# Performance work log

Hardware: AMD Instinct MI355X
Metric: run time of the kernel (lower is better)

Reference implementation:

```python
import jax, jax.numpy as jnp
import numpy as np

B, L, D = 2, 2048, 2048
H, KV, HD = 16, 8, 128
EPS = 1e-5
ROPE_BASE = 10000.0
SCALING_ALPHA = 1.0
SCALE = HD ** -0.5


def setup_inputs() -> dict:
    key = jax.random.key(0)
    ks = jax.random.split(key, 5)
    s = 0.02  # weight init scale
    return {
        "x": jax.random.normal(ks[0], (B, L, D), jnp.float32),
        "wq": jax.random.normal(ks[1], (D, H * HD), jnp.float32) * s,
        "wk": jax.random.normal(ks[2], (D, KV * HD), jnp.float32) * s,
        "wv": jax.random.normal(ks[3], (D, KV * HD), jnp.float32) * s,
        "wo": jax.random.normal(ks[4], (H * HD, D), jnp.float32) * s,
        "qn_w": jnp.ones((HD,), jnp.float32),
        "kn_w": jnp.ones((HD,), jnp.float32),
    }


def _rope(t):
    # t: [B, h, L, HD]. DynamicNTKAlpha base scaling (alpha=1 -> no-op).
    base = ROPE_BASE * SCALING_ALPHA ** (HD / (HD - 2))
    # NOTE: source uses base**(+i/d) (no negative exponent) -- kept faithful.
    freqs = base ** (jnp.arange(0, HD, 2, dtype=jnp.float32) / HD)  # [HD/2]
    pos = jnp.arange(t.shape[-2], dtype=jnp.float32)                # [L]
    angles = pos[:, None] * freqs[None, :]                          # [L, HD/2]
    cos, sin = jnp.cos(angles), jnp.sin(angles)
    x1, x2 = t[..., : HD // 2], t[..., HD // 2 :]
    return jnp.concatenate([x1 * cos - x2 * sin, x2 * cos + x1 * sin], axis=-1)


def _rmsnorm(t, w):
    return t * jax.lax.rsqrt(jnp.mean(t * t, axis=-1, keepdims=True) + EPS) * w


def reference(x, wq, wk, wv, wo, qn_w, kn_w):
    b, l, _ = x.shape
    q = (x @ wq).reshape(b, l, H, HD).transpose(0, 2, 1, 3)   # [B,H,L,HD]
    k = (x @ wk).reshape(b, l, KV, HD).transpose(0, 2, 1, 3)  # [B,KV,L,HD]
    v = (x @ wv).reshape(b, l, KV, HD).transpose(0, 2, 1, 3)
    q = _rmsnorm(_rope(q), qn_w)
    k = _rmsnorm(_rope(k), kn_w)
    # GQA: expand KV heads to match query heads
    rep = H // KV
    k = jnp.repeat(k, rep, axis=1)  # [B,H,L,HD]
    v = jnp.repeat(v, rep, axis=1)
    scores = jnp.einsum("bhqd,bhkd->bhqk", q, k) * SCALE
    probs = jax.nn.softmax(scores, axis=-1)
    out = jnp.einsum("bhqk,bhkd->bhqd", probs, v)             # [B,H,L,HD]
    out = out.transpose(0, 2, 1, 3).reshape(b, l, H * HD)
    return out @ wo
```

## Files before the change

kernel.cpp:

```cpp
#include <hip/hip_runtime.h>
#include <math.h>

#define BB 2
#define LL 2048
#define DD 2048
#define HH 16
#define KVH 8
#define HDIM 128
#define SCALE_F 0.08838834764831845f
#define EPS_F 1e-5f
#define LOG2E 1.4426950408889634f
#define SMAX_F 17.0f
#define QKVW 4096

typedef unsigned short u16;
typedef __attribute__((ext_vector_type(8))) short short8;
typedef __attribute__((ext_vector_type(4))) float f32x4;
typedef __attribute__((ext_vector_type(16))) float f32x16;

#define MFMA16(a, b, c) __builtin_amdgcn_mfma_f32_16x16x32_bf16((a), (b), (c), 0, 0, 0)
#define MFMA32(a, b, c) __builtin_amdgcn_mfma_f32_32x32x16_bf16((a), (b), (c), 0, 0, 0)

__device__ __forceinline__ float b2f(u16 u) {
    union { unsigned int i; float f; } x;
    x.i = ((unsigned int)u) << 16;
    return x.f;
}
__device__ __forceinline__ u16 f2b(float f) {
    unsigned int x = __float_as_uint(f);
    unsigned int r = x + 0x7FFFu + ((x >> 16) & 1u);
    return (u16)(r >> 16);
}
__device__ __forceinline__ unsigned cvtpk(float lo, float hi) {
    unsigned r;
    asm("v_cvt_pk_bf16_f32 %0, %1, %2" : "=v"(r) : "v"(lo), "v"(hi));
    return r;
}
__device__ __forceinline__ void pl32swap(unsigned &a, unsigned &b) {
    asm("v_permlane32_swap_b32 %0, %1" : "+v"(a), "+v"(b));
}
__device__ __forceinline__ void g2l(const u16* g, u16* l) {
    __builtin_amdgcn_global_load_lds(
        (const __attribute__((address_space(1))) unsigned int*)g,
        (__attribute__((address_space(3))) unsigned int*)l, 16, 0, 0);
}

__global__ __launch_bounds__(256) void prep_kernel(const float* __restrict__ x,
                                                   u16* __restrict__ xb,
                                                   const float* __restrict__ wq,
                                                   const float* __restrict__ wk,
                                                   const float* __restrict__ wv,
                                                   const float* __restrict__ wo,
                                                   u16* __restrict__ wqkvT,
                                                   u16* __restrict__ woT,
                                                   float* __restrict__ ct,
                                                   float* __restrict__ st) {
    __shared__ u16 t[64 * 65];
    const int blk = blockIdx.x, tid = threadIdx.x;
    if (blk < 8192) {
        int i = (blk * 256 + tid) * 4;
        float4 v = *(const float4*)(x + i);
        unsigned int p0 = (unsigned int)f2b(v.x) | ((unsigned int)f2b(v.y) << 16);
        unsigned int p1 = (unsigned int)f2b(v.z) | ((unsigned int)f2b(v.w) << 16);
        uint2 pk; pk.x = p0; pk.y = p1;
        *(uint2*)(xb + i) = pk;
    } else if (blk < 11264) {
        int j = blk - 8192;
        const float* in; u16* out; int C, bx, by;
        if (j < 1024)      { in = wq; out = wqkvT;                      C = 2048; bx = j & 31; by = j >> 5; }
        else if (j < 1536) { j -= 1024; in = wk; out = wqkvT + (size_t)2048 * DD; C = 1024; bx = j & 15; by = j >> 4; }
        else if (j < 2048) { j -= 1536; in = wv; out = wqkvT + (size_t)3072 * DD; C = 1024; bx = j & 15; by = j >> 4; }
        else               { j -= 2048; in = wo; out = woT;                      C = 2048; bx = j & 31; by = j >> 5; }
        int c0 = bx * 64, r0 = by * 64;
#pragma unroll
        for (int i = 0; i < 16; i++) {
            int idx = tid + i * 256;
            int r = idx >> 6, c = idx & 63;
            t[r * 65 + c] = f2b(in[(size_t)(r0 + r) * C + c0 + c]);
        }
        __syncthreads();
#pragma unroll
        for (int i = 0; i < 16; i++) {
            int idx = tid + i * 256;
            int r = idx >> 6, c = idx & 63;
            out[(size_t)(c0 + r) * DD + r0 + c] = t[c * 65 + r];
        }
    } else {
        int i = (blk - 11264) * 256 + tid;
        int pos = i >> 6, d = i & 63;
        float freq = (float)pow(10000.0, (double)d * (1.0 / 64.0));
        float ang = (float)pos * freq;
        double a = (double)ang;
        ct[i] = (float)cos(a);
        st[i] = (float)sin(a);
    }
}

__global__ __launch_bounds__(256) void gemm_bt(const u16* __restrict__ A,
                                               const u16* __restrict__ Bt,
                                               u16* __restrict__ C, int M, int N, int K) {
    __shared__ __align__(16) u16 As[128 * 64];
    __shared__ __align__(16) u16 Bs[128 * 64];
    const int tid = threadIdx.x;
    const int w = tid >> 6, lane = tid & 63;
    const int lm = lane & 15, lq = lane >> 4;
    const int bn0 = blockIdx.x * 128, bm0 = blockIdx.y * 128;
    const int wm = (w >> 1) * 64, wn = (w & 1) * 64;

    f32x4 acc[4][4];
#pragma unroll
    for (int i = 0; i < 4; i++)
#pragma unroll
        for (int j = 0; j < 4; j++) acc[i][j] = (f32x4){0.f, 0.f, 0.f, 0.f};

    const int srow = lane >> 3;
    const int sgr = (lane & 7) ^ (srow & 7);
    const u16* ga = A + (size_t)(bm0 + w * 32 + srow) * K + sgr * 8;
    const u16* gb = Bt + (size_t)(bn0 + w * 32 + srow) * K + sgr * 8;
    u16* lA = &As[(w * 32) * 64];
    u16* lB = &Bs[(w * 32) * 64];

    for (int k0 = 0; k0 < K; k0 += 64) {
        __syncthreads();
#pragma unroll
        for (int ch = 0; ch < 4; ch++)
            g2l(ga + (size_t)(ch * 8) * K + k0, lA + ch * 8 * 64);
#pragma unroll
        for (int ch = 0; ch < 4; ch++)
            g2l(gb + (size_t)(ch * 8) * K + k0, lB + ch * 8 * 64);
        __syncthreads();

#pragma unroll
        for (int sub = 0; sub < 2; sub++) {
            short8 af[4], bf[4];
#pragma unroll
            for (int mt = 0; mt < 4; mt++) {
                int row = wm + mt * 16 + lm;
                af[mt] = *(const short8*)(&As[row * 64 + ((sub * 4 + lq) ^ (lm & 7)) * 8]);
            }
#pragma unroll
            for (int nt = 0; nt < 4; nt++) {
                int row = wn + nt * 16 + lm;
                bf[nt] = *(const short8*)(&Bs[row * 64 + ((sub * 4 + lq) ^ (lm & 7)) * 8]);
            }
#pragma unroll
            for (int mt = 0; mt < 4; mt++)
#pragma unroll
                for (int nt = 0; nt < 4; nt++) acc[mt][nt] = MFMA16(af[mt], bf[nt], acc[mt][nt]);
        }
    }

#pragma unroll
    for (int mt = 0; mt < 4; mt++)
#pragma unroll
        for (int nt = 0; nt < 4; nt++)
#pragma unroll
            for (int r = 0; r < 4; r++) {
                int row = bm0 + wm + mt * 16 + lq * 4 + r;
                int col = bn0 + wn + nt * 16 + lm;
                C[(size_t)row * N + col] = f2b(acc[mt][nt][r]);
            }
}

__global__ __launch_bounds__(256) void gemm_bt_o(const u16* __restrict__ A,
                                                 const u16* __restrict__ Bt,
                                                 float* __restrict__ C, int M, int N, int K) {
    __shared__ __align__(16) u16 As[64 * 64];
    __shared__ __align__(16) u16 Bs[128 * 64];
    const int tid = threadIdx.x;
    const int w = tid >> 6, lane = tid & 63;
    const int lm = lane & 15, lq = lane >> 4;
    const int bn0 = blockIdx.x * 128, bm0 = blockIdx.y * 64;
    const int wm = (w >> 1) * 32, wn = (w & 1) * 64;

    f32x4 acc[2][4];
#pragma unroll
    for (int i = 0; i < 2; i++)
#pragma unroll
        for (int j = 0; j < 4; j++) acc[i][j] = (f32x4){0.f, 0.f, 0.f, 0.f};

    const int srow = lane >> 3;
    const int sgr = (lane & 7) ^ (srow & 7);
    const u16* ga = A + (size_t)(bm0 + w * 16 + srow) * K + sgr * 8;
    const u16* gb = Bt + (size_t)(bn0 + w * 32 + srow) * K + sgr * 8;
    u16* lA = &As[(w * 16) * 64];
    u16* lB = &Bs[(w * 32) * 64];

    for (int k0 = 0; k0 < K; k0 += 64) {
        __syncthreads();
#pragma unroll
        for (int ch = 0; ch < 2; ch++)
            g2l(ga + (size_t)(ch * 8) * K + k0, lA + ch * 8 * 64);
#pragma unroll
        for (int ch = 0; ch < 4; ch++)
            g2l(gb + (size_t)(ch * 8) * K + k0, lB + ch * 8 * 64);
        __syncthreads();

#pragma unroll
        for (int sub = 0; sub < 2; sub++) {
            short8 af[2], bf[4];
#pragma unroll
            for (int mt = 0; mt < 2; mt++) {
                int row = wm + mt * 16 + lm;
                af[mt] = *(const short8*)(&As[row * 64 + ((sub * 4 + lq) ^ (lm & 7)) * 8]);
            }
#pragma unroll
            for (int nt = 0; nt < 4; nt++) {
                int row = wn + nt * 16 + lm;
                bf[nt] = *(const short8*)(&Bs[row * 64 + ((sub * 4 + lq) ^ (lm & 7)) * 8]);
            }
#pragma unroll
            for (int mt = 0; mt < 2; mt++)
#pragma unroll
                for (int nt = 0; nt < 4; nt++) acc[mt][nt] = MFMA16(af[mt], bf[nt], acc[mt][nt]);
        }
    }

#pragma unroll
    for (int mt = 0; mt < 2; mt++)
#pragma unroll
        for (int nt = 0; nt < 4; nt++)
#pragma unroll
            for (int r = 0; r < 4; r++) {
                int row = bm0 + wm + mt * 16 + lq * 4 + r;
                int col = bn0 + wn + nt * 16 + lm;
                C[(size_t)row * N + col] = acc[mt][nt][r];
            }
}

__global__ __launch_bounds__(256) void ropetv_kernel(u16* __restrict__ qkv,
                                                     u16* __restrict__ vt,
                                                     const float* __restrict__ qw,
                                                     const float* __restrict__ kw,
                                                     const float* __restrict__ ct,
                                                     const float* __restrict__ st) {
    __shared__ u16 t[64 * 65];
    const int blk = blockIdx.x, tid = threadIdx.x;
    if (blk < 24576) {
        int slot = blk * 4 + (tid >> 6);
        int lane = tid & 63;
        int hh = slot % (HH + KVH);
        int row = slot / (HH + KVH);
        int pos = row & (LL - 1);

        u16* base = qkv + (size_t)row * QKVW + hh * HDIM;
        const float* w = (hh < HH) ? qw : kw;

        float x1 = b2f(base[lane]), x2 = b2f(base[lane + 64]);
        float c = ct[pos * 64 + lane], s = st[pos * 64 + lane];
        float r1 = x1 * c - x2 * s;
        float r2 = x2 * c + x1 * s;
        float ss = r1 * r1 + r2 * r2;
#pragma unroll
        for (int m = 1; m < 64; m <<= 1) ss += __shfl_xor(ss, m, 64);
        float sc = 1.0f / sqrtf(ss * (1.0f / 128.0f) + EPS_F);
        base[lane] = f2b(r1 * sc * w[lane]);
        base[lane + 64] = f2b(r2 * sc * w[lane + 64]);
    } else {
        int j = blk - 24576;
        int bx = j & 31, by = (j >> 5) & 1, bg = j >> 6;
        int l0 = bx * 64, d0 = by * 64;
        int b = bg >> 3, g = bg & 7;
        const u16* src = qkv + (size_t)b * LL * QKVW + 3072 + g * HDIM;
        u16* dst = vt + (size_t)bg * HDIM * LL;
#pragma unroll
        for (int i = 0; i < 16; i++) {
            int idx = tid + i * 256;
            int r = idx >> 6, c = idx & 63;
            t[r * 65 + c] = src[(size_t)(l0 + r) * QKVW + d0 + c];
        }
        __syncthreads();
#pragma unroll
        for (int i = 0; i < 16; i++) {
            int idx = tid + i * 256;
            int r = idx >> 6, c = idx & 63;
            dst[(size_t)(d0 + r) * LL + l0 + c] = t[c * 65 + r];
        }
    }
}

__global__ __launch_bounds__(256, 2) void attn_kernel(const u16* __restrict__ qkv,
                                                      const u16* __restrict__ vt,
                                                      u16* __restrict__ ob) {
    __shared__ __align__(16) u16 Kt[2][64 * 128];
    __shared__ __align__(16) u16 Vt[2][128 * 64];

    const int tid = threadIdx.x, w = tid >> 6, lane = tid & 63;
    const int l31 = lane & 31, lh = lane >> 5;
    const int q0 = blockIdx.x * 128;
    const int bh = blockIdx.y, b = bh >> 4, hd = bh & 15, g = hd >> 1;

    const u16* kbase = qkv + (size_t)b * LL * QKVW + 2048 + g * HDIM;
    const u16* vtbase = vt + (size_t)(b * KVH + g) * HDIM * LL;

    const int krl = lane >> 4, kgl = lane & 15;
    const int vrl = lane >> 3, vgl = lane & 7;

#define STAGE(tt, bi) do {                                                   \
        _Pragma("unroll")                                                    \
        for (int ch = 0; ch < 4; ch++) {                                     \
            int r_ = w * 16 + ch * 4 + krl;                                  \
            int gc_ = kgl ^ (r_ & 15);                                       \
            g2l(kbase + (size_t)((tt) * 64 + r_) * QKVW + gc_ * 8,           \
                &Kt[bi][(w * 16 + ch * 4) * 128]);                           \
        }                                                                    \
        _Pragma("unroll")                                                    \
        for (int ch = 0; ch < 4; ch++) {                                     \
            int r_ = w * 32 + ch * 8 + vrl;                                  \
            int gc_ = vgl ^ (r_ & 7);                                        \
            g2l(vtbase + (size_t)r_ * LL + (tt) * 64 + gc_ * 8,              \
                &Vt[bi][(w * 32 + ch * 8) * 64]);                            \
        }                                                                    \
    } while (0)

    const int qrow = q0 + w * 32 + l31;
    short8 aq[8];
    {
        const u16* qp = qkv + (size_t)(b * LL + qrow) * QKVW + hd * HDIM + lh * 8;
#pragma unroll
        for (int kk = 0; kk < 8; kk++) aq[kk] = *(const short8*)(qp + kk * 16);
    }

    f32x16 o[4];
#pragma unroll
    for (int i = 0; i < 4; i++)
#pragma unroll
        for (int r = 0; r < 16; r++) o[i][r] = 0.f;
    float psum = 0.f;
    const float SC2 = SCALE_F * LOG2E;

    STAGE(0, 0);
    __syncthreads();

    int cur = 0;
    for (int t = 0; t < LL / 64; t++) {
        if (t + 1 < LL / 64) STAGE(t + 1, cur ^ 1);

        f32x16 s[2];
#pragma unroll
        for (int kt = 0; kt < 2; kt++)
#pragma unroll
            for (int r = 0; r < 16; r++) s[kt][r] = 0.f;
        __builtin_amdgcn_s_setprio(1);
#pragma unroll
        for (int kk = 0; kk < 8; kk++) {
#pragma unroll
            for (int kt = 0; kt < 2; kt++) {
                int key = kt * 32 + l31;
                int gg = (kk * 2 + lh) ^ (key & 15);
                short8 kf = *(const short8*)(&Kt[cur][key * 128 + gg * 8]);
                s[kt] = MFMA32(kf, aq[kk], s[kt]);
            }
        }
        __builtin_amdgcn_s_setprio(0);

        unsigned pw[4][4];
#pragma unroll
        for (int kt = 0; kt < 2; kt++) {
            float p[16];
#pragma unroll
            for (int r = 0; r < 16; r++) {
                p[r] = exp2f(fmaf(s[kt][r], SC2, -SMAX_F));
                psum += p[r];
            }
#pragma unroll
            for (int half = 0; half < 2; half++) {
                int kc = kt * 2 + half, qb = half * 8;
                unsigned c0 = cvtpk(p[qb + 0], p[qb + 1]);
                unsigned c1 = cvtpk(p[qb + 2], p[qb + 3]);
                unsigned c2 = cvtpk(p[qb + 4], p[qb + 5]);
                unsigned c3 = cvtpk(p[qb + 6], p[qb + 7]);
                pl32swap(c0, c2);
                pl32swap(c1, c3);
                pw[kc][0] = c0; pw[kc][1] = c1; pw[kc][2] = c2; pw[kc][3] = c3;
            }
        }

        __builtin_amdgcn_s_setprio(1);
#pragma unroll
        for (int kc = 0; kc < 4; kc++) {
            union { unsigned u[4]; short8 s8; } pu;
#pragma unroll
            for (int i = 0; i < 4; i++) pu.u[i] = pw[kc][i];
#pragma unroll
            for (int dn = 0; dn < 4; dn++) {
                int d = dn * 32 + l31;
                int gv = ((kc * 2 + lh) ^ (d & 7)) * 8;
                short8 bv = *(const short8*)(&Vt[cur][d * 64 + gv]);
                o[dn] = MFMA32(pu.s8, bv, o[dn]);
            }
        }
        __builtin_amdgcn_s_setprio(0);

        __syncthreads();
        cur ^= 1;
    }
#undef STAGE

    psum += __shfl_xor(psum, 32, 64);
    float inv = 1.0f / psum;
    float invr[16];
#pragma unroll
    for (int r = 0; r < 16; r++) {
        int row = (r & 3) + 8 * (r >> 2) + 4 * lh;
        invr[r] = __shfl(inv, row, 32);
    }

    u16* obase = ob + (size_t)(b * LL + q0 + w * 32) * (HH * HDIM) + hd * HDIM;
#pragma unroll
    for (int dn = 0; dn < 4; dn++)
#pragma unroll
        for (int r = 0; r < 16; r++) {
            int row = (r & 3) + 8 * (r >> 2) + 4 * lh;
            obase[(size_t)row * (HH * HDIM) + dn * 32 + l31] = f2b(o[dn][r] * invr[r]);
        }
}

extern "C" void kernel_launch(void* const* d_in, const int* in_sizes, int n_in,
                              void* d_out, int out_size, void* d_ws, size_t ws_size,
                              hipStream_t stream) {
    const float* x  = (const float*)d_in[0];
    const float* wq = (const float*)d_in[1];
    const float* wk = (const float*)d_in[2];
    const float* wv = (const float*)d_in[3];
    const float* wo = (const float*)d_in[4];
    const float* qn = (const float*)d_in[5];
    const float* kn = (const float*)d_in[6];

    u16* ws = (u16*)d_ws;
    const size_t SZ_X = (size_t)BB * LL * DD;
    u16* xb    = ws;
    u16* qkv   = xb + SZ_X;
    u16* wqkvT = qkv + (size_t)BB * LL * QKVW;
    u16* woT   = wqkvT + (size_t)QKVW * DD;
    float* ct  = (float*)(woT + (size_t)DD * DD);
    float* st  = ct + (size_t)LL * 64;
    u16* att = xb;
    u16* vt  = wqkvT;

    prep_kernel<<<dim3(11776), dim3(256), 0, stream>>>(x, xb, wq, wk, wv, wo,
                                                       wqkvT, woT, ct, st);
    gemm_bt<<<dim3(QKVW / 128, BB * LL / 128), dim3(256), 0, stream>>>(xb, wqkvT, qkv, BB * LL, QKVW, DD);
    ropetv_kernel<<<dim3(25600), dim3(256), 0, stream>>>(qkv, vt, qn, kn, ct, st);
    attn_kernel<<<dim3(LL / 128, BB * HH), dim3(256), 0, stream>>>(qkv, vt, att);
    gemm_bt_o<<<dim3(DD / 128, BB * LL / 64), dim3(256), 0, stream>>>(att, woT, (float*)d_out, BB * LL, DD, DD);
}
```

Measured before the change: 362.7 us.

## Split attention key tiles across warps with 64-query blocks and merge partial outputs

The attention kernel now processes 64 query rows per block instead of 128. Warps are split into two query halves and two key halves, and each warp computes one 32-key subtile. The partial outputs and row sums are combined through shared memory at the end. V is now single-buffered while K stays double-buffered, with explicit vmcnt waits and barriers, which cuts shared memory so three blocks can fit per CU and doubles the grid. The cost is an extra in-block barrier per tile, a final reduction through LDS, and reloading K and V for twice as many blocks.

```diff
diff --git a/kernel.cpp b/kernel.cpp
--- a/kernel.cpp
+++ b/kernel.cpp
@@ -279,15 +279,16 @@
     }
 }
 
-__global__ __launch_bounds__(256, 2) void attn_kernel(const u16* __restrict__ qkv,
+__global__ __launch_bounds__(256, 3) void attn_kernel(const u16* __restrict__ qkv,
                                                       const u16* __restrict__ vt,
                                                       u16* __restrict__ ob) {
-    __shared__ __align__(16) u16 Kt[2][64 * 128];
-    __shared__ __align__(16) u16 Vt[2][128 * 64];
+    __shared__ __align__(16) u16 SM[2 * 64 * 128 + 128 * 64];
+    u16* Vt = SM + 2 * 64 * 128;
 
     const int tid = threadIdx.x, w = tid >> 6, lane = tid & 63;
     const int l31 = lane & 31, lh = lane >> 5;
-    const int q0 = blockIdx.x * 128;
+    const int qh = w & 1, kh = w >> 1;
+    const int q0 = blockIdx.x * 64;
     const int bh = blockIdx.y, b = bh >> 4, hd = bh & 15, g = hd >> 1;
 
     const u16* kbase = qkv + (size_t)b * LL * QKVW + 2048 + g * HDIM;
@@ -296,24 +297,26 @@
     const int krl = lane >> 4, kgl = lane & 15;
     const int vrl = lane >> 3, vgl = lane & 7;
 
-#define STAGE(tt, bi) do {                                                   \
+#define STAGEK(tt, bi) do {                                                  \
         _Pragma("unroll")                                                    \
         for (int ch = 0; ch < 4; ch++) {                                     \
             int r_ = w * 16 + ch * 4 + krl;                                  \
             int gc_ = kgl ^ (r_ & 15);                                       \
             g2l(kbase + (size_t)((tt) * 64 + r_) * QKVW + gc_ * 8,           \
-                &Kt[bi][(w * 16 + ch * 4) * 128]);                           \
+                SM + (bi) * 8192 + (w * 16 + ch * 4) * 128);                 \
         }                                                                    \
+    } while (0)
+#define STAGEV(tt) do {                                                      \
         _Pragma("unroll")                                                    \
         for (int ch = 0; ch < 4; ch++) {                                     \
             int r_ = w * 32 + ch * 8 + vrl;                                  \
             int gc_ = vgl ^ (r_ & 7);                                        \
             g2l(vtbase + (size_t)r_ * LL + (tt) * 64 + gc_ * 8,              \
-                &Vt[bi][(w * 32 + ch * 8) * 64]);                            \
+                Vt + (w * 32 + ch * 8) * 64);                                \
         }                                                                    \
     } while (0)
 
-    const int qrow = q0 + w * 32 + l31;
+    const int qrow = q0 + qh * 32 + l31;
     short8 aq[8];
     {
         const u16* qp = qkv + (size_t)(b * LL + qrow) * QKVW + hd * HDIM + lh * 8;
@@ -328,92 +331,114 @@
         for (int r = 0; r < 16; r++) o[i][r] = 0.f;
     float psum = 0.f;
     const float SC2 = SCALE_F * LOG2E;
-
-    STAGE(0, 0);
-    __syncthreads();
-
-    int cur = 0;
+    const f32x16 fz = {};
+
+    STAGEK(0, 0);
+    asm volatile("s_waitcnt vmcnt(0)" ::: "memory");
+    __builtin_amdgcn_s_barrier();
+
     for (int t = 0; t < LL / 64; t++) {
-        if (t + 1 < LL / 64) STAGE(t + 1, cur ^ 1);
-
-        f32x16 s[2];
-#pragma unroll
-        for (int kt = 0; kt < 2; kt++)
-#pragma unroll
-            for (int r = 0; r < 16; r++) s[kt][r] = 0.f;
+        const int cur = t & 1;
+        const u16* Kc = SM + cur * 8192;
+        STAGEV(t);
+        STAGEK((t + 1) & (LL / 64 - 1), cur ^ 1);
+
+        const int key = kh * 32 + l31;
+        f32x16 s;
         __builtin_amdgcn_s_setprio(1);
-#pragma unroll
-        for (int kk = 0; kk < 8; kk++) {
-#pragma unroll
-            for (int kt = 0; kt < 2; kt++) {
-                int key = kt * 32 + l31;
-                int gg = (kk * 2 + lh) ^ (key & 15);
-                short8 kf = *(const short8*)(&Kt[cur][key * 128 + gg * 8]);
-                s[kt] = MFMA32(kf, aq[kk], s[kt]);
-            }
+        {
+            int gg = lh ^ (key & 15);
+            short8 kf = *(const short8*)(&Kc[key * 128 + gg * 8]);
+            s = MFMA32(kf, aq[0], fz);
+        }
+#pragma unroll
+        for (int kk = 1; kk < 8; kk++) {
+            int gg = (kk * 2 + lh) ^ (key & 15);
+            short8 kf = *(const short8*)(&Kc[key * 128 + gg * 8]);
+            s = MFMA32(kf, aq[kk], s);
         }
         __builtin_amdgcn_s_setprio(0);
 
-        unsigned pw[4][4];
-#pragma unroll
-        for (int kt = 0; kt < 2; kt++) {
-            float p[16];
-#pragma unroll
-            for (int r = 0; r < 16; r++) {
-                p[r] = exp2f(fmaf(s[kt][r], SC2, -SMAX_F));
-                psum += p[r];
-            }
-#pragma unroll
-            for (int half = 0; half < 2; half++) {
-                int kc = kt * 2 + half, qb = half * 8;
-                unsigned c0 = cvtpk(p[qb + 0], p[qb + 1]);
-                unsigned c1 = cvtpk(p[qb + 2], p[qb + 3]);
-                unsigned c2 = cvtpk(p[qb + 4], p[qb + 5]);
-                unsigned c3 = cvtpk(p[qb + 6], p[qb + 7]);
-                pl32swap(c0, c2);
-                pl32swap(c1, c3);
-                pw[kc][0] = c0; pw[kc][1] = c1; pw[kc][2] = c2; pw[kc][3] = c3;
-            }
-        }
+        float p[16];
+#pragma unroll
+        for (int r = 0; r < 16; r++) {
+            p[r] = __builtin_amdgcn_exp2f(fmaf(s[r], SC2, -SMAX_F));
+            psum += p[r];
+        }
+        unsigned pw[2][4];
+#pragma unroll
+        for (int half = 0; half < 2; half++) {
+            int qb = half * 8;
+            unsigned c0 = cvtpk(p[qb + 0], p[qb + 1]);
+            unsigned c1 = cvtpk(p[qb + 2], p[qb + 3]);
+            unsigned c2 = cvtpk(p[qb + 4], p[qb + 5]);
+            unsigned c3 = cvtpk(p[qb + 6], p[qb + 7]);
+            pl32swap(c0, c2);
+            pl32swap(c1, c3);
+            pw[half][0] = c0; pw[half][1] = c1; pw[half][2] = c2; pw[half][3] = c3;
+        }
+
+        asm volatile("s_waitcnt vmcnt(4)" ::: "memory");
+        __builtin_amdgcn_s_barrier();
 
         __builtin_amdgcn_s_setprio(1);
 #pragma unroll
-        for (int kc = 0; kc < 4; kc++) {
+        for (int kcl = 0; kcl < 2; kcl++) {
+            int kc = kh * 2 + kcl;
             union { unsigned u[4]; short8 s8; } pu;
 #pragma unroll
-            for (int i = 0; i < 4; i++) pu.u[i] = pw[kc][i];
+            for (int i = 0; i < 4; i++) pu.u[i] = pw[kcl][i];
 #pragma unroll
             for (int dn = 0; dn < 4; dn++) {
                 int d = dn * 32 + l31;
                 int gv = ((kc * 2 + lh) ^ (d & 7)) * 8;
-                short8 bv = *(const short8*)(&Vt[cur][d * 64 + gv]);
+                short8 bv = *(const short8*)(&Vt[d * 64 + gv]);
                 o[dn] = MFMA32(pu.s8, bv, o[dn]);
             }
         }
         __builtin_amdgcn_s_setprio(0);
 
-        __syncthreads();
-        cur ^= 1;
-    }
-#undef STAGE
+        asm volatile("s_waitcnt vmcnt(0)" ::: "memory");
+        __builtin_amdgcn_s_barrier();
+    }
+#undef STAGEK
+#undef STAGEV
 
     psum += __shfl_xor(psum, 32, 64);
-    float inv = 1.0f / psum;
-    float invr[16];
-#pragma unroll
-    for (int r = 0; r < 16; r++) {
-        int row = (r & 3) + 8 * (r >> 2) + 4 * lh;
-        invr[r] = __shfl(inv, row, 32);
-    }
-
-    u16* obase = ob + (size_t)(b * LL + q0 + w * 32) * (HH * HDIM) + hd * HDIM;
-#pragma unroll
-    for (int dn = 0; dn < 4; dn++)
+
+    __syncthreads();
+    float* xo = (float*)SM;
+    float* xp = xo + 2 * 64 * 68;
+    if (kh == 1) {
+        float* dst = xo + (qh * 64 + lane) * 68;
+#pragma unroll
+        for (int dn = 0; dn < 4; dn++)
+#pragma unroll
+            for (int r = 0; r < 16; r += 4)
+                *(f32x4*)(dst + dn * 16 + r) =
+                    (f32x4){o[dn][r], o[dn][r + 1], o[dn][r + 2], o[dn][r + 3]};
+        xp[qh * 64 + lane] = psum;
+    }
+    __syncthreads();
+    if (kh == 0) {
+        const float* src = xo + (qh * 64 + lane) * 68;
+        float inv = 1.0f / (psum + xp[qh * 64 + lane]);
+        float invr[16];
 #pragma unroll
         for (int r = 0; r < 16; r++) {
             int row = (r & 3) + 8 * (r >> 2) + 4 * lh;
-            obase[(size_t)row * (HH * HDIM) + dn * 32 + l31] = f2b(o[dn][r] * invr[r]);
-        }
+            invr[r] = __shfl(inv, row, 32);
+        }
+        u16* obase = ob + (size_t)(b * LL + q0 + qh * 32) * (HH * HDIM) + hd * HDIM;
+#pragma unroll
+        for (int dn = 0; dn < 4; dn++)
+#pragma unroll
+            for (int r = 0; r < 16; r++) {
+                int row = (r & 3) + 8 * (r >> 2) + 4 * lh;
+                float v = o[dn][r] + src[dn * 16 + r];
+                obase[(size_t)row * (HH * HDIM) + dn * 32 + l31] = f2b(v * invr[r]);
+            }
+    }
 }
 
 extern "C" void kernel_launch(void* const* d_in, const int* in_sizes, int n_in,
@@ -442,6 +467,6 @@
                                                        wqkvT, woT, ct, st);
     gemm_bt<<<dim3(QKVW / 128, BB * LL / 128), dim3(256), 0, stream>>>(xb, wqkvT, qkv, BB * LL, QKVW, DD);
     ropetv_kernel<<<dim3(25600), dim3(256), 0, stream>>>(qkv, vt, qn, kn, ct, st);
-    attn_kernel<<<dim3(LL / 128, BB * HH), dim3(256), 0, stream>>>(qkv, vt, att);
+    attn_kernel<<<dim3(LL / 64, BB * HH), dim3(256), 0, stream>>>(qkv, vt, att);
     gemm_bt_o<<<dim3(DD / 128, BB * LL / 64), dim3(256), 0, stream>>>(att, woT, (float*)d_out, BB * LL, DD, DD);
 }
```

Result: no change. 367.2 us (+1.2%).
